# Kernel tuning notes

Hardware: AMD Instinct MI355X
Metric: run time of the kernel (lower is better)

The kernel has to match this reference:

```python
import jax, jax.numpy as jnp
import numpy as np

B, S, D_MODEL, H = 8, 2048, 256, 4
DEPTH = D_MODEL // H


def setup_inputs() -> dict:
    key = jax.random.key(0)
    ks = jax.random.split(key, 9)
    std = 1.0 / np.sqrt(D_MODEL)
    return {
        "v": jax.random.normal(ks[0], (B, S, D_MODEL), jnp.float32),
        "k": jax.random.normal(ks[1], (B, S, D_MODEL), jnp.float32),
        "q": jax.random.normal(ks[2], (B, S, D_MODEL), jnp.float32),
        "mask": jax.random.uniform(ks[3], (B, 1, 1, S), jnp.float32),
        "wq": jax.random.normal(ks[4], (D_MODEL, D_MODEL), jnp.float32) * std,
        "bq": jnp.zeros((D_MODEL,), jnp.float32),
        "wk": jax.random.normal(ks[5], (D_MODEL, D_MODEL), jnp.float32) * std,
        "bk": jnp.zeros((D_MODEL,), jnp.float32),
        "wv": jax.random.normal(ks[6], (D_MODEL, D_MODEL), jnp.float32) * std,
        "bv": jnp.zeros((D_MODEL,), jnp.float32),
        "wo": jax.random.normal(ks[7], (D_MODEL, D_MODEL), jnp.float32) * std,
        "bo": jnp.zeros((D_MODEL,), jnp.float32),
    }


def _split_heads(x):
    # [B, S, d_model] -> [B, H, S, depth]
    b, s, _ = x.shape
    return x.reshape(b, s, H, DEPTH).transpose(0, 2, 1, 3)


def reference(v, k, q, mask, wq, bq, wk, bk, wv, bv, wo, bo):
    qh = _split_heads(q @ wq + bq)   # [B,H,Sq,depth]
    kh = _split_heads(k @ wk + bk)   # [B,H,Sk,depth]
    vh = _split_heads(v @ wv + bv)   # [B,H,Sk,depth]
    scale = 1.0 / jnp.sqrt(jnp.asarray(DEPTH, jnp.float32))
    logits = jnp.einsum("bhqd,bhkd->bhqk", qh, kh) * scale
    logits = logits + mask * (-1e9)
    attn = jax.nn.softmax(logits, axis=-1)
    out = jnp.einsum("bhqk,bhkd->bhqd", attn, vh)  # [B,H,Sq,depth]
    concat = out.transpose(0, 2, 1, 3).reshape(out.shape[0], -1, D_MODEL)
    return concat @ wo + bo
```

## Files before the change

### kernel.cpp

```cpp
#include <hip/hip_runtime.h>

#define DEV __device__ __forceinline__

typedef __attribute__((ext_vector_type(4))) float f32x4;
typedef __bf16 bf16_t;
typedef __attribute__((ext_vector_type(4))) bf16_t bf16x4;
typedef __attribute__((ext_vector_type(8))) bf16_t bf16x8;
typedef __attribute__((ext_vector_type(8))) unsigned short us8;
typedef __attribute__((ext_vector_type(4))) unsigned short us4;


DEV unsigned short f2bf(float f) {
  bf16_t h = (bf16_t)f;
  return __builtin_bit_cast(unsigned short, h);
}

DEV void gl2lds16(const void* g, void* l) {
  __builtin_amdgcn_global_load_lds(
      (const __attribute__((address_space(1))) unsigned int*)g,
      (__attribute__((address_space(3))) unsigned int*)l, 16, 0, 0);
}

DEV f32x4 mfma16(bf16x8 a, bf16x8 b, f32x4 c) {
  return __builtin_amdgcn_mfma_f32_16x16x32_bf16(a, b, c, 0, 0, 0);
}

__global__ __launch_bounds__(256) void prep_w(
    const float* __restrict__ wq, const float* __restrict__ wk,
    const float* __restrict__ wv, const float* __restrict__ wo,
    const float* __restrict__ mask,
    unsigned short* __restrict__ wt, float* __restrict__ mc,
    int* __restrict__ gidx, int* __restrict__ nct) {
  const int t = threadIdx.x;
  if (blockIdx.x < 64) {
    __shared__ float T[64 * 65];
    const int mat = blockIdx.x >> 4, tn = (blockIdx.x >> 2) & 3, tk = blockIdx.x & 3;
    const int n0 = tn * 64, k0 = tk * 64;
    const float* W = (mat == 0) ? wq : (mat == 1) ? wk : (mat == 2) ? wv : wo;
    const int r0 = t >> 4, c = (t & 15) * 4;
#pragma unroll
    for (int i = 0; i < 4; ++i) {
      int rr = r0 + i * 16;
      f32x4 x = *(const f32x4*)(W + (k0 + rr) * 256 + n0 + c);
#pragma unroll
      for (int j = 0; j < 4; ++j) T[(c + j) * 65 + rr] = x[j];
    }
    __syncthreads();
#pragma unroll
    for (int i = 0; i < 2; ++i) {
      int u = t + i * 256;
      int n = u >> 3, seg = u & 7;
      us8 pk;
#pragma unroll
      for (int j = 0; j < 8; ++j) pk[j] = f2bf(T[n * 65 + seg * 8 + j]);
      *(us8*)(&wt[mat * 65536 + (n0 + n) * 256 + k0 + seg * 8]) = pk;
    }
  } else {
    __shared__ float redf[256];
    __shared__ int redi[256];
    const int b = blockIdx.x - 64;
    const float* mr = mask + b * 2048;
    f32x4 x0 = *(const f32x4*)(mr + t * 8);
    f32x4 x1 = *(const f32x4*)(mr + t * 8 + 4);
    float mv[8];
#pragma unroll
    for (int j = 0; j < 4; ++j) { mv[j] = x0[j]; mv[4 + j] = x1[j]; }
    float mn = mv[0];
#pragma unroll
    for (int j = 1; j < 8; ++j) mn = fminf(mn, mv[j]);
    redf[t] = mn;
    __syncthreads();
    for (int s = 128; s > 0; s >>= 1) {
      if (t < s) redf[t] = fminf(redf[t], redf[t + s]);
      __syncthreads();
    }
    const float minb = redf[0];
    const float thr = minb + 1.45e-6f;
    int myc = 0;
#pragma unroll
    for (int j = 0; j < 8; ++j) myc += (mv[j] < thr) ? 1 : 0;
    redi[t] = myc;
    __syncthreads();
    for (int s = 1; s < 256; s <<= 1) {
      int add = (t >= s) ? redi[t - s] : 0;
      __syncthreads();
      redi[t] += add;
      __syncthreads();
    }
    int pos = redi[t] - myc;
    const int cntb = redi[255];
#pragma unroll
    for (int j = 0; j < 8; ++j)
      if (mv[j] < thr) {
        gidx[b * 2048 + pos] = t * 8 + j;
        mc[b * 2048 + pos] = (mv[j] - minb) * -1.442695041e9f;
        ++pos;
      }
    if (t == 0) {
      int nt = (cntb + 63) >> 6;
      if (nt < 1) nt = 1;
      nct[b] = nt;
      for (int j = cntb; j < nt * 64; ++j) {
        gidx[b * 2048 + j] = 0;
        mc[b * 2048 + j] = -1.0e30f;
      }
    }
  }
}

__global__ __launch_bounds__(256, 4) void gemm_q(
    const float* __restrict__ Aq, const float* __restrict__ bq,
    const unsigned short* __restrict__ wt,
    unsigned short* __restrict__ Qh) {
  __shared__ __align__(16) unsigned short At[32 * 64];
  __shared__ __align__(16) unsigned short Bt[256 * 64];
  const unsigned short* WT = wt;
  const int t = threadIdx.x, lane = t & 63, w = t >> 6;
  const int lr = lane & 15, lg = lane >> 4;
  const int lx = lr & 7;
  const int m0 = blockIdx.x * 32;

  const int as_row = t >> 3, as_seg = t & 7;
  const float* agp = Aq + (m0 + as_row) * 256 + as_seg * 8;

  f32x4 acc[2][4] = {};

  for (int j = 0; j < 4; ++j) {
    const int k0 = j * 64;
#pragma unroll
    for (int i = 0; i < 8; ++i) {
      int u = t + i * 256;
      int row = u >> 3, g = (u & 7) ^ (row & 7);
      gl2lds16(WT + row * 256 + k0 + g * 8, &Bt[u * 8]);
    }
    {
      f32x4 x0 = *(const f32x4*)(agp + k0);
      f32x4 x1 = *(const f32x4*)(agp + k0 + 4);
      us8 pk;
#pragma unroll
      for (int jj = 0; jj < 4; ++jj) { pk[jj] = f2bf(x0[jj]); pk[jj + 4] = f2bf(x1[jj]); }
      *(us8*)(&At[(as_row << 6) + ((as_seg ^ (as_row & 7)) << 3)]) = pk;
    }
    __syncthreads();

#pragma unroll
    for (int ds = 0; ds < 2; ++ds) {
      const int ku = (ds << 2) | lg;
      const int phys = (ku ^ lx) << 3;
      bf16x8 af[2], bfr[4];
#pragma unroll
      for (int m = 0; m < 2; ++m)
        af[m] = *(const bf16x8*)(&At[((m * 16 + lr) << 6) + phys]);
#pragma unroll
      for (int cg = 0; cg < 4; ++cg)
        bfr[cg] = *(const bf16x8*)(&Bt[((w * 64 + cg * 16 + lr) << 6) + phys]);
#pragma unroll
      for (int m = 0; m < 2; ++m)
#pragma unroll
        for (int cg = 0; cg < 4; ++cg)
          acc[m][cg] = mfma16(af[m], bfr[cg], acc[m][cg]);
    }
    __syncthreads();
  }

  const int b = m0 >> 11, s0 = m0 & 2047;
  const int bh = b * 4 + w;
#pragma unroll
  for (int cg = 0; cg < 4; ++cg) {
    int d = cg * 16 + lr;
    float bb = bq[w * 64 + d];
#pragma unroll
    for (int m = 0; m < 2; ++m) {
      int sb = s0 + m * 16 + lg * 4;
#pragma unroll
      for (int r = 0; r < 4; ++r)
        Qh[(bh * 2048 + sb + r) * 64 + d] = f2bf(acc[m][cg][r] + bb);
    }
  }
}

__global__ __launch_bounds__(512) void gemm_kv(
    const float* __restrict__ kin, const float* __restrict__ vin,
    const float* __restrict__ bk, const float* __restrict__ bv,
    const unsigned short* __restrict__ wt, const int* __restrict__ gidx,
    const int* __restrict__ nct,
    unsigned short* __restrict__ Khc, unsigned short* __restrict__ VhcT) {
  const int gt = blockIdx.x, b = blockIdx.y, p = blockIdx.z;
  if (gt >= nct[b]) return;

  __shared__ __align__(16) unsigned short At[64 * 256];
  __shared__ __align__(16) unsigned short Bt[256 * 256];
  const float* A    = p ? vin : kin;
  const float* bias = p ? bv : bk;
  const unsigned short* WT = wt + (p ? 2 : 1) * 65536;
  const int t = threadIdx.x, lane = t & 63, w = t >> 6;
  const int lr = lane & 15, lg = lane >> 4;
  const int lx = lr & 7;
  const int* gi = gidx + b * 2048 + gt * 64;

#pragma unroll
  for (int i = 0; i < 16; ++i) {
    int u = t + i * 512;
    int row = u >> 5, un = u & 31;
    int g = (un & 24) | ((un & 7) ^ (row & 7));
    gl2lds16(WT + row * 256 + g * 8, &Bt[u * 8]);
  }
  {
    const int row = t >> 3, seg = (t & 7) * 4;
    const int srow = gi[row];
    const float* src = A + (b * 2048 + srow) * 256 + seg * 8;
#pragma unroll
    for (int j = 0; j < 4; ++j) {
      f32x4 x0 = *(const f32x4*)(src + j * 8);
      f32x4 x1 = *(const f32x4*)(src + j * 8 + 4);
      us8 pk;
#pragma unroll
      for (int jj = 0; jj < 4; ++jj) { pk[jj] = f2bf(x0[jj]); pk[jj + 4] = f2bf(x1[jj]); }
      int un = seg + j;
      *(us8*)(&At[row * 256 + (((un & 24) | ((un & 7) ^ (row & 7))) << 3)]) = pk;
    }
  }
  __syncthreads();

  f32x4 acc[4][2] = {};
#pragma unroll
  for (int ds = 0; ds < 8; ++ds) {
    const int ku = ds * 4 + lg;
    const int phys = ((ku & 24) | ((ku & 7) ^ lx)) << 3;
    bf16x8 af[4], bfr[2];
#pragma unroll
    for (int m = 0; m < 4; ++m)
      af[m] = *(const bf16x8*)(&At[(m * 16 + lr) * 256 + phys]);
#pragma unroll
    for (int n = 0; n < 2; ++n)
      bfr[n] = *(const bf16x8*)(&Bt[(w * 32 + n * 16 + lr) * 256 + phys]);
#pragma unroll
    for (int m = 0; m < 4; ++m)
#pragma unroll
      for (int n = 0; n < 2; ++n)
        acc[m][n] = mfma16(af[m], bfr[n], acc[m][n]);
  }

#pragma unroll
  for (int n = 0; n < 2; ++n) {
    int col = w * 32 + n * 16 + lr;
    float bb = bias[col];
    int h = col >> 6, d = col & 63;
    int bh = b * 4 + h;
#pragma unroll
    for (int m = 0; m < 4; ++m) {
      int pos = gt * 64 + m * 16 + lg * 4;
      if (p) {
        us4 o;
#pragma unroll
        for (int r = 0; r < 4; ++r) o[r] = f2bf(acc[m][n][r] + bb);
        *(us4*)(&VhcT[(bh * 64 + d) * 2048 + pos]) = o;
      } else {
#pragma unroll
        for (int r = 0; r < 4; ++r)
          Khc[(bh * 2048 + pos + r) * 64 + d] = f2bf(acc[m][n][r] + bb);
      }
    }
  }
}

__global__ __launch_bounds__(512) void attn_out(
    const unsigned short* __restrict__ Qh, const unsigned short* __restrict__ Kh,
    const unsigned short* __restrict__ VhT, const float* __restrict__ mc,
    const int* __restrict__ nct, const unsigned short* __restrict__ wt,
    const float* __restrict__ bo, float* __restrict__ out) {
  __shared__ __align__(16) unsigned short L[81920];
  const int b = blockIdx.y;
  const int q0 = blockIdx.x * 64;
  const int t = threadIdx.x, lane = t & 63, w = t >> 6;
  const int lr = lane & 15, lg = lane >> 4;
  const int h = w >> 1, ch = w & 1;
  const int bh = b * 4 + h;
  const float* mrow = mc + b * 2048;
  const int lx = lr & 7;
  const int lgh = lg >> 1, lgo = (lg & 1) * 4;

  bf16x8 qf[2][2];
#pragma unroll
  for (int cc = 0; cc < 2; ++cc)
#pragma unroll
    for (int ds = 0; ds < 2; ++ds)
      qf[cc][ds] = *(const bf16x8*)(Qh + (bh * 2048 + q0 + ch * 32 + cc * 16 + lr) * 64 + ds * 32 + lg * 8);

  f32x4 accO[2][4] = {};
  float mrun[2] = {-3.0e38f, -3.0e38f}, lrun[2] = {0.f, 0.f};

#define STAGE(buf, kv)                                                        \
  {                                                                           \
    _Pragma("unroll")                                                         \
    for (int i = 0; i < 4; ++i) {                                             \
      int u = t + i * 512;                                                    \
      int hh = u >> 9, vv = u & 511;                                          \
      int row = vv >> 3, g = (vv & 7) ^ (row & 7);                            \
      gl2lds16(Kh + ((b * 4 + hh) * 2048 + (kv) + row) * 64 + g * 8,          \
               &L[((buf) * 16384 + hh * 4096 + vv * 8)]);                     \
      gl2lds16(VhT + ((b * 4 + hh) * 64 + row) * 2048 + (kv) + g * 8,         \
               &L[(32768 + (buf) * 16384 + hh * 4096 + vv * 8)]);             \
    }                                                                         \
  }

  const int cnt = nct[b];
  STAGE(0, 0)
  __syncthreads();
  int cur = 0;

  for (int j = 0; j < cnt; ++j) {
    const int kv0 = j * 64;
    if (j + 1 < cnt) STAGE(cur ^ 1, kv0 + 64)

    const int kb_base = cur * 16384 + h * 4096;
    const int vb_base = 32768 + kb_base;

#pragma unroll
    for (int cc = 0; cc < 2; ++cc) {
      f32x4 accS[4] = {};
      __builtin_amdgcn_s_setprio(1);
#pragma unroll
      for (int kb = 0; kb < 4; ++kb)
#pragma unroll
        for (int ds = 0; ds < 2; ++ds) {
          bf16x8 kf = *(const bf16x8*)(&L[kb_base + (((kb * 16 + lr) << 3) | (((ds << 2) | lg) ^ lx)) * 8]);
          accS[kb] = mfma16(kf, qf[cc][ds], accS[kb]);
        }
      __builtin_amdgcn_s_setprio(0);

      f32x4 sv[4];
#pragma unroll
      for (int kb = 0; kb < 4; ++kb) {
        f32x4 mk = *(const f32x4*)(mrow + kv0 + kb * 16 + lg * 4);
        sv[kb] = accS[kb] * 0.1803368801f + mk;
      }
      float mx0 = fmaxf(fmaxf(sv[0][0], sv[0][1]), fmaxf(sv[0][2], sv[0][3]));
      float mx1 = fmaxf(fmaxf(sv[1][0], sv[1][1]), fmaxf(sv[1][2], sv[1][3]));
      float mx2 = fmaxf(fmaxf(sv[2][0], sv[2][1]), fmaxf(sv[2][2], sv[2][3]));
      float mx3 = fmaxf(fmaxf(sv[3][0], sv[3][1]), fmaxf(sv[3][2], sv[3][3]));
      float mx = fmaxf(fmaxf(mx0, mx1), fmaxf(mx2, mx3));
      mx = fmaxf(mx, __shfl_xor(mx, 16));
      mx = fmaxf(mx, __shfl_xor(mx, 32));
      float mnew = fmaxf(mrun[cc], mx);
      float al = __builtin_amdgcn_exp2f(mrun[cc] - mnew);
      mrun[cc] = mnew;

      float px[4][4];
      float lsum = 0.f;
#pragma unroll
      for (int kb = 0; kb < 4; ++kb) {
        float s = 0.f;
#pragma unroll
        for (int r = 0; r < 4; ++r) {
          px[kb][r] = __builtin_amdgcn_exp2f(sv[kb][r] - mnew);
          s += px[kb][r];
        }
        lsum += s;
      }
      lsum += __shfl_xor(lsum, 16);
      lsum += __shfl_xor(lsum, 32);
      lrun[cc] = lrun[cc] * al + lsum;
#pragma unroll
      for (int db = 0; db < 4; ++db) accO[cc][db] *= al;

      bf16x8 pf[2];
#pragma unroll
      for (int ks = 0; ks < 2; ++ks) {
        bf16x8 p;
#pragma unroll
        for (int r = 0; r < 4; ++r) {
          p[r]     = (bf16_t)px[2 * ks][r];
          p[r + 4] = (bf16_t)px[2 * ks + 1][r];
        }
        pf[ks] = p;
      }

      __builtin_amdgcn_s_setprio(1);
#pragma unroll
      for (int ks = 0; ks < 2; ++ks)
#pragma unroll
        for (int db = 0; db < 4; ++db) {
          int row = db * 16 + lr;
          int u0 = (row << 3) | (((ks << 2) | lgh) ^ lx);
          int u1 = (row << 3) | (((ks << 2) | 2 | lgh) ^ lx);
          bf16x4 v0 = *(const bf16x4*)(&L[vb_base + u0 * 8 + lgo]);
          bf16x4 v1 = *(const bf16x4*)(&L[vb_base + u1 * 8 + lgo]);
          bf16x8 vf = __builtin_shufflevector(v0, v1, 0, 1, 2, 3, 4, 5, 6, 7);
          accO[cc][db] = mfma16(vf, pf[ks], accO[cc][db]);
        }
      __builtin_amdgcn_s_setprio(0);
    }

    __syncthreads();
    cur ^= 1;
  }
#undef STAGE

#pragma unroll
  for (int cc = 0; cc < 2; ++cc) {
    const float inv = __builtin_amdgcn_rcpf(lrun[cc]);
    const int row = ch * 32 + cc * 16 + lr;
#pragma unroll
    for (int db = 0; db < 4; ++db) {
      us4 o;
#pragma unroll
      for (int r = 0; r < 4; ++r) o[r] = f2bf(accO[cc][db][r] * inv);
      int un = h * 8 + db * 2 + (lg >> 1);
      int phys = (un & 24) | ((un & 7) ^ (row & 7));
      *(us4*)(&L[65536 + row * 256 + phys * 8 + (lg & 1) * 4]) = o;
    }
  }
  __syncthreads();

  const unsigned short* WT = wt + 3 * 65536;
#pragma unroll
  for (int i = 0; i < 16; ++i) {
    int u = t + i * 512;
    int row = u >> 5, un = u & 31;
    int g = (un & 24) | ((un & 7) ^ (row & 7));
    gl2lds16(WT + row * 256 + g * 8, &L[u * 8]);
  }
  __syncthreads();

  f32x4 acc[4][2] = {};
#pragma unroll
  for (int ds = 0; ds < 8; ++ds) {
    const int ku = ds * 4 + lg;
    const int phys = ((ku & 24) | ((ku & 7) ^ lx)) << 3;
    bf16x8 af[4], bfr[2];
#pragma unroll
    for (int m = 0; m < 4; ++m)
      af[m] = *(const bf16x8*)(&L[65536 + (m * 16 + lr) * 256 + phys]);
#pragma unroll
    for (int n = 0; n < 2; ++n)
      bfr[n] = *(const bf16x8*)(&L[(w * 32 + n * 16 + lr) * 256 + phys]);
#pragma unroll
    for (int m = 0; m < 4; ++m)
#pragma unroll
      for (int n = 0; n < 2; ++n)
        acc[m][n] = mfma16(af[m], bfr[n], acc[m][n]);
  }

#pragma unroll
  for (int cgi = 0; cgi < 2; ++cgi) {
    int col = w * 32 + cgi * 16 + lr;
    float bb = bo[col];
#pragma unroll
    for (int m = 0; m < 4; ++m) {
      int rowg = b * 2048 + q0 + m * 16 + lg * 4;
#pragma unroll
      for (int r = 0; r < 4; ++r)
        out[(rowg + r) * 256 + col] = acc[m][cgi][r] + bb;
    }
  }
}

extern "C" void kernel_launch(void* const* d_in, const int* in_sizes, int n_in,
                              void* d_out, int out_size, void* d_ws, size_t ws_size,
                              hipStream_t stream) {
  const float* v    = (const float*)d_in[0];
  const float* k    = (const float*)d_in[1];
  const float* q    = (const float*)d_in[2];
  const float* mask = (const float*)d_in[3];
  const float* wq   = (const float*)d_in[4];
  const float* bq   = (const float*)d_in[5];
  const float* wk   = (const float*)d_in[6];
  const float* bk   = (const float*)d_in[7];
  const float* wv   = (const float*)d_in[8];
  const float* bv   = (const float*)d_in[9];
  const float* wo   = (const float*)d_in[10];
  const float* bo   = (const float*)d_in[11];
  float* out = (float*)d_out;
  char* ws = (char*)d_ws;

  unsigned short* wt  = (unsigned short*)(ws);
  float*          mc  = (float*)(ws + 524288);
  int*            gi  = (int*)(ws + 589824);
  int*            nc  = (int*)(ws + 655360);
  unsigned short* Qh  = (unsigned short*)(ws + 659456);
  unsigned short* Khc = (unsigned short*)(ws + 659456 + 8388608);
  unsigned short* VhT = (unsigned short*)(ws + 659456 + 2 * 8388608);

  prep_w<<<dim3(72), dim3(256), 0, stream>>>(wq, wk, wv, wo, mask, wt, mc, gi, nc);
  gemm_q<<<dim3(512), dim3(256), 0, stream>>>(q, bq, wt, Qh);
  gemm_kv<<<dim3(32, 8, 2), dim3(512), 0, stream>>>(k, v, bk, bv, wt, gi, nc, Khc, VhT);
  attn_out<<<dim3(32, 8), dim3(512), 0, stream>>>(Qh, Khc, VhT, mc, nc, wt, bo, out);
}
```

Baseline: 48.26 us.

## Merge Q and compacted K/V projection GEMMs into one launch with K-chunked tiling

Combines the separate Q projection and K/V projection kernels into a single launch with a 2-row grid. Q blocks keep their old path, while K/V blocks are re-tiled to 256 threads and stream the weight in four 64-wide K chunks instead of staging the full 256x256 weight in LDS. The aim is to remove one launch and its serialization gap, cut the K/V kernel's large LDS footprint so more blocks fit per CU, and let the Q and K/V work overlap. In exchange each K/V block now syncs four times and has more accumulator registers, and the launch bound of 4 blocks per SM for the Q path is dropped.

```diff
diff --git a/kernel.cpp b/kernel.cpp
--- a/kernel.cpp
+++ b/kernel.cpp
@@ -108,157 +108,147 @@
   }
 }
 
-__global__ __launch_bounds__(256, 4) void gemm_q(
-    const float* __restrict__ Aq, const float* __restrict__ bq,
-    const unsigned short* __restrict__ wt,
-    unsigned short* __restrict__ Qh) {
-  __shared__ __align__(16) unsigned short At[32 * 64];
+__global__ __launch_bounds__(256) void gemm_qkv(
+    const float* __restrict__ qin, const float* __restrict__ kin,
+    const float* __restrict__ vin,
+    const float* __restrict__ bq, const float* __restrict__ bk,
+    const float* __restrict__ bv,
+    const unsigned short* __restrict__ wt, const int* __restrict__ gidx,
+    const int* __restrict__ nct,
+    unsigned short* __restrict__ Qh, unsigned short* __restrict__ Khc,
+    unsigned short* __restrict__ VhcT) {
+  __shared__ __align__(16) unsigned short At[64 * 64];
   __shared__ __align__(16) unsigned short Bt[256 * 64];
-  const unsigned short* WT = wt;
   const int t = threadIdx.x, lane = t & 63, w = t >> 6;
   const int lr = lane & 15, lg = lane >> 4;
   const int lx = lr & 7;
-  const int m0 = blockIdx.x * 32;
-
-  const int as_row = t >> 3, as_seg = t & 7;
-  const float* agp = Aq + (m0 + as_row) * 256 + as_seg * 8;
-
-  f32x4 acc[2][4] = {};
-
-  for (int j = 0; j < 4; ++j) {
-    const int k0 = j * 64;
-#pragma unroll
-    for (int i = 0; i < 8; ++i) {
-      int u = t + i * 256;
-      int row = u >> 3, g = (u & 7) ^ (row & 7);
-      gl2lds16(WT + row * 256 + k0 + g * 8, &Bt[u * 8]);
-    }
-    {
-      f32x4 x0 = *(const f32x4*)(agp + k0);
-      f32x4 x1 = *(const f32x4*)(agp + k0 + 4);
-      us8 pk;
-#pragma unroll
-      for (int jj = 0; jj < 4; ++jj) { pk[jj] = f2bf(x0[jj]); pk[jj + 4] = f2bf(x1[jj]); }
-      *(us8*)(&At[(as_row << 6) + ((as_seg ^ (as_row & 7)) << 3)]) = pk;
-    }
-    __syncthreads();
-
-#pragma unroll
-    for (int ds = 0; ds < 2; ++ds) {
-      const int ku = (ds << 2) | lg;
-      const int phys = (ku ^ lx) << 3;
-      bf16x8 af[2], bfr[4];
-#pragma unroll
-      for (int m = 0; m < 2; ++m)
-        af[m] = *(const bf16x8*)(&At[((m * 16 + lr) << 6) + phys]);
-#pragma unroll
-      for (int cg = 0; cg < 4; ++cg)
-        bfr[cg] = *(const bf16x8*)(&Bt[((w * 64 + cg * 16 + lr) << 6) + phys]);
-#pragma unroll
-      for (int m = 0; m < 2; ++m)
+
+  if (blockIdx.y == 0) {
+    const int m0 = blockIdx.x * 32;
+    const int as_row = t >> 3, as_seg = t & 7;
+    const float* agp = qin + (m0 + as_row) * 256 + as_seg * 8;
+
+    f32x4 acc[2][4] = {};
+    for (int j = 0; j < 4; ++j) {
+      const int k0 = j * 64;
+#pragma unroll
+      for (int i = 0; i < 8; ++i) {
+        int u = t + i * 256;
+        int row = u >> 3, g = (u & 7) ^ (row & 7);
+        gl2lds16(wt + row * 256 + k0 + g * 8, &Bt[u * 8]);
+      }
+      {
+        f32x4 x0 = *(const f32x4*)(agp + k0);
+        f32x4 x1 = *(const f32x4*)(agp + k0 + 4);
+        us8 pk;
+#pragma unroll
+        for (int jj = 0; jj < 4; ++jj) { pk[jj] = f2bf(x0[jj]); pk[jj + 4] = f2bf(x1[jj]); }
+        *(us8*)(&At[(as_row << 6) + ((as_seg ^ (as_row & 7)) << 3)]) = pk;
+      }
+      __syncthreads();
+#pragma unroll
+      for (int ds = 0; ds < 2; ++ds) {
+        const int ku = (ds << 2) | lg;
+        const int phys = (ku ^ lx) << 3;
+        bf16x8 af[2], bfr[4];
+#pragma unroll
+        for (int m = 0; m < 2; ++m)
+          af[m] = *(const bf16x8*)(&At[((m * 16 + lr) << 6) + phys]);
 #pragma unroll
         for (int cg = 0; cg < 4; ++cg)
-          acc[m][cg] = mfma16(af[m], bfr[cg], acc[m][cg]);
-    }
-    __syncthreads();
-  }
-
-  const int b = m0 >> 11, s0 = m0 & 2047;
-  const int bh = b * 4 + w;
-#pragma unroll
-  for (int cg = 0; cg < 4; ++cg) {
-    int d = cg * 16 + lr;
-    float bb = bq[w * 64 + d];
-#pragma unroll
-    for (int m = 0; m < 2; ++m) {
-      int sb = s0 + m * 16 + lg * 4;
-#pragma unroll
-      for (int r = 0; r < 4; ++r)
-        Qh[(bh * 2048 + sb + r) * 64 + d] = f2bf(acc[m][cg][r] + bb);
-    }
-  }
-}
-
-__global__ __launch_bounds__(512) void gemm_kv(
-    const float* __restrict__ kin, const float* __restrict__ vin,
-    const float* __restrict__ bk, const float* __restrict__ bv,
-    const unsigned short* __restrict__ wt, const int* __restrict__ gidx,
-    const int* __restrict__ nct,
-    unsigned short* __restrict__ Khc, unsigned short* __restrict__ VhcT) {
-  const int gt = blockIdx.x, b = blockIdx.y, p = blockIdx.z;
-  if (gt >= nct[b]) return;
-
-  __shared__ __align__(16) unsigned short At[64 * 256];
-  __shared__ __align__(16) unsigned short Bt[256 * 256];
-  const float* A    = p ? vin : kin;
-  const float* bias = p ? bv : bk;
-  const unsigned short* WT = wt + (p ? 2 : 1) * 65536;
-  const int t = threadIdx.x, lane = t & 63, w = t >> 6;
-  const int lr = lane & 15, lg = lane >> 4;
-  const int lx = lr & 7;
-  const int* gi = gidx + b * 2048 + gt * 64;
-
-#pragma unroll
-  for (int i = 0; i < 16; ++i) {
-    int u = t + i * 512;
-    int row = u >> 5, un = u & 31;
-    int g = (un & 24) | ((un & 7) ^ (row & 7));
-    gl2lds16(WT + row * 256 + g * 8, &Bt[u * 8]);
-  }
-  {
-    const int row = t >> 3, seg = (t & 7) * 4;
-    const int srow = gi[row];
-    const float* src = A + (b * 2048 + srow) * 256 + seg * 8;
-#pragma unroll
+          bfr[cg] = *(const bf16x8*)(&Bt[((w * 64 + cg * 16 + lr) << 6) + phys]);
+#pragma unroll
+        for (int m = 0; m < 2; ++m)
+#pragma unroll
+          for (int cg = 0; cg < 4; ++cg)
+            acc[m][cg] = mfma16(af[m], bfr[cg], acc[m][cg]);
+      }
+      __syncthreads();
+    }
+
+    const int b = m0 >> 11, s0 = m0 & 2047;
+    const int bh = b * 4 + w;
+#pragma unroll
+    for (int cg = 0; cg < 4; ++cg) {
+      int d = cg * 16 + lr;
+      float bb = bq[w * 64 + d];
+#pragma unroll
+      for (int m = 0; m < 2; ++m) {
+        int sb = s0 + m * 16 + lg * 4;
+#pragma unroll
+        for (int r = 0; r < 4; ++r)
+          Qh[(bh * 2048 + sb + r) * 64 + d] = f2bf(acc[m][cg][r] + bb);
+      }
+    }
+  } else {
+    const int x = blockIdx.x;
+    const int p = x >> 8, b = (x >> 5) & 7, gt = x & 31;
+    if (gt >= nct[b]) return;
+    const float* A    = p ? vin : kin;
+    const float* bias = p ? bv : bk;
+    const unsigned short* WT = wt + (p ? 2 : 1) * 65536;
+    const int* gi = gidx + b * 2048 + gt * 64;
+
+    f32x4 acc[4][4] = {};
     for (int j = 0; j < 4; ++j) {
-      f32x4 x0 = *(const f32x4*)(src + j * 8);
-      f32x4 x1 = *(const f32x4*)(src + j * 8 + 4);
-      us8 pk;
-#pragma unroll
-      for (int jj = 0; jj < 4; ++jj) { pk[jj] = f2bf(x0[jj]); pk[jj + 4] = f2bf(x1[jj]); }
-      int un = seg + j;
-      *(us8*)(&At[row * 256 + (((un & 24) | ((un & 7) ^ (row & 7))) << 3)]) = pk;
-    }
-  }
-  __syncthreads();
-
-  f32x4 acc[4][2] = {};
-#pragma unroll
-  for (int ds = 0; ds < 8; ++ds) {
-    const int ku = ds * 4 + lg;
-    const int phys = ((ku & 24) | ((ku & 7) ^ lx)) << 3;
-    bf16x8 af[4], bfr[2];
-#pragma unroll
-    for (int m = 0; m < 4; ++m)
-      af[m] = *(const bf16x8*)(&At[(m * 16 + lr) * 256 + phys]);
-#pragma unroll
-    for (int n = 0; n < 2; ++n)
-      bfr[n] = *(const bf16x8*)(&Bt[(w * 32 + n * 16 + lr) * 256 + phys]);
-#pragma unroll
-    for (int m = 0; m < 4; ++m)
-#pragma unroll
-      for (int n = 0; n < 2; ++n)
-        acc[m][n] = mfma16(af[m], bfr[n], acc[m][n]);
-  }
-
-#pragma unroll
-  for (int n = 0; n < 2; ++n) {
-    int col = w * 32 + n * 16 + lr;
-    float bb = bias[col];
-    int h = col >> 6, d = col & 63;
-    int bh = b * 4 + h;
-#pragma unroll
-    for (int m = 0; m < 4; ++m) {
-      int pos = gt * 64 + m * 16 + lg * 4;
-      if (p) {
-        us4 o;
-#pragma unroll
-        for (int r = 0; r < 4; ++r) o[r] = f2bf(acc[m][n][r] + bb);
-        *(us4*)(&VhcT[(bh * 64 + d) * 2048 + pos]) = o;
-      } else {
-#pragma unroll
-        for (int r = 0; r < 4; ++r)
-          Khc[(bh * 2048 + pos + r) * 64 + d] = f2bf(acc[m][n][r] + bb);
+      const int k0 = j * 64;
+#pragma unroll
+      for (int i = 0; i < 8; ++i) {
+        int u = t + i * 256;
+        int row = u >> 3, g = (u & 7) ^ (row & 7);
+        gl2lds16(WT + row * 256 + k0 + g * 8, &Bt[u * 8]);
+      }
+#pragma unroll
+      for (int i = 0; i < 2; ++i) {
+        int slot = t + i * 256;
+        int row = slot >> 3, seg = slot & 7;
+        const float* src = A + (b * 2048 + gi[row]) * 256 + k0 + seg * 8;
+        f32x4 x0 = *(const f32x4*)src;
+        f32x4 x1 = *(const f32x4*)(src + 4);
+        us8 pk;
+#pragma unroll
+        for (int jj = 0; jj < 4; ++jj) { pk[jj] = f2bf(x0[jj]); pk[jj + 4] = f2bf(x1[jj]); }
+        *(us8*)(&At[(row << 6) + ((seg ^ (row & 7)) << 3)]) = pk;
+      }
+      __syncthreads();
+#pragma unroll
+      for (int ds = 0; ds < 2; ++ds) {
+        const int ku = (ds << 2) | lg;
+        const int phys = (ku ^ lx) << 3;
+        bf16x8 af[4], bfr[4];
+#pragma unroll
+        for (int m = 0; m < 4; ++m)
+          af[m] = *(const bf16x8*)(&At[((m * 16 + lr) << 6) + phys]);
+#pragma unroll
+        for (int cg = 0; cg < 4; ++cg)
+          bfr[cg] = *(const bf16x8*)(&Bt[((w * 64 + cg * 16 + lr) << 6) + phys]);
+#pragma unroll
+        for (int m = 0; m < 4; ++m)
+#pragma unroll
+          for (int cg = 0; cg < 4; ++cg)
+            acc[m][cg] = mfma16(af[m], bfr[cg], acc[m][cg]);
+      }
+      __syncthreads();
+    }
+
+    const int bh = b * 4 + w;
+#pragma unroll
+    for (int cg = 0; cg < 4; ++cg) {
+      int d = cg * 16 + lr;
+      float bb = bias[w * 64 + d];
+#pragma unroll
+      for (int m = 0; m < 4; ++m) {
+        int pos = gt * 64 + m * 16 + lg * 4;
+        if (p) {
+          us4 o;
+#pragma unroll
+          for (int r = 0; r < 4; ++r) o[r] = f2bf(acc[m][cg][r] + bb);
+          *(us4*)(&VhcT[(bh * 64 + d) * 2048 + pos]) = o;
+        } else {
+#pragma unroll
+          for (int r = 0; r < 4; ++r)
+            Khc[(bh * 2048 + pos + r) * 64 + d] = f2bf(acc[m][cg][r] + bb);
+        }
       }
     }
   }
@@ -483,7 +473,6 @@
   unsigned short* VhT = (unsigned short*)(ws + 659456 + 2 * 8388608);
 
   prep_w<<<dim3(72), dim3(256), 0, stream>>>(wq, wk, wv, wo, mask, wt, mc, gi, nc);
-  gemm_q<<<dim3(512), dim3(256), 0, stream>>>(q, bq, wt, Qh);
-  gemm_kv<<<dim3(32, 8, 2), dim3(512), 0, stream>>>(k, v, bk, bv, wt, gi, nc, Khc, VhT);
+  gemm_qkv<<<dim3(512, 2), dim3(256), 0, stream>>>(q, k, v, bq, bk, bv, wt, gi, nc, Qh, Khc, VhT);
   attn_out<<<dim3(32, 8), dim3(512), 0, stream>>>(Qh, Khc, VhT, mc, nc, wt, bo, out);
 }
```

Result: faster. 41.33 us (-14.4%).

## Fuse Q projection into attention and compute compacted K/V rows in prep kernel

Applied to the files above, without the earlier changes.

Removes the separate Q GEMM and K/V GEMM kernels. The Q projection is now computed per block inside the attention kernel from fp32 inputs staged through LDS, so the Qh workspace round trip disappears. K/V projections for the few mask-selected key rows are computed with scalar FMA loops in the prep kernel. This cuts two launches and intermediate traffic. The trade-offs are that the prep kernel now does serial per-row work, and the padded K/V rows beyond the selected count are no longer written, so they hold uninitialized data.

```diff
diff --git a/kernel.cpp b/kernel.cpp
--- a/kernel.cpp
+++ b/kernel.cpp
@@ -25,52 +25,54 @@
   return __builtin_amdgcn_mfma_f32_16x16x32_bf16(a, b, c, 0, 0, 0);
 }
 
-__global__ __launch_bounds__(256) void prep_w(
-    const float* __restrict__ wq, const float* __restrict__ wk,
-    const float* __restrict__ wv, const float* __restrict__ wo,
+__global__ __launch_bounds__(512) void prep_kv(
+    const float* __restrict__ wq, const float* __restrict__ wo,
+    const float* __restrict__ wk, const float* __restrict__ wv,
+    const float* __restrict__ bk, const float* __restrict__ bv,
     const float* __restrict__ mask,
+    const float* __restrict__ kin, const float* __restrict__ vin,
     unsigned short* __restrict__ wt, float* __restrict__ mc,
-    int* __restrict__ gidx, int* __restrict__ nct) {
+    int* __restrict__ nct,
+    unsigned short* __restrict__ Khc, unsigned short* __restrict__ VhcT) {
   const int t = threadIdx.x;
-  if (blockIdx.x < 64) {
+  if (blockIdx.x < 32) {
     __shared__ float T[64 * 65];
     const int mat = blockIdx.x >> 4, tn = (blockIdx.x >> 2) & 3, tk = blockIdx.x & 3;
     const int n0 = tn * 64, k0 = tk * 64;
-    const float* W = (mat == 0) ? wq : (mat == 1) ? wk : (mat == 2) ? wv : wo;
-    const int r0 = t >> 4, c = (t & 15) * 4;
-#pragma unroll
-    for (int i = 0; i < 4; ++i) {
-      int rr = r0 + i * 16;
-      f32x4 x = *(const f32x4*)(W + (k0 + rr) * 256 + n0 + c);
-#pragma unroll
-      for (int j = 0; j < 4; ++j) T[(c + j) * 65 + rr] = x[j];
+    const float* W = (mat == 0) ? wq : wo;
+    if (t < 256) {
+      const int r0 = t >> 4, c = (t & 15) * 4;
+#pragma unroll
+      for (int i = 0; i < 4; ++i) {
+        int rr = r0 + i * 16;
+        f32x4 x = *(const f32x4*)(W + (k0 + rr) * 256 + n0 + c);
+#pragma unroll
+        for (int j = 0; j < 4; ++j) T[(c + j) * 65 + rr] = x[j];
+      }
     }
     __syncthreads();
-#pragma unroll
-    for (int i = 0; i < 2; ++i) {
-      int u = t + i * 256;
-      int n = u >> 3, seg = u & 7;
-      us8 pk;
-#pragma unroll
-      for (int j = 0; j < 8; ++j) pk[j] = f2bf(T[n * 65 + seg * 8 + j]);
-      *(us8*)(&wt[mat * 65536 + (n0 + n) * 256 + k0 + seg * 8]) = pk;
+    if (t < 256) {
+#pragma unroll
+      for (int i = 0; i < 2; ++i) {
+        int u = t + i * 256;
+        int n = u >> 3, seg = u & 7;
+        us8 pk;
+#pragma unroll
+        for (int j = 0; j < 8; ++j) pk[j] = f2bf(T[n * 65 + seg * 8 + j]);
+        *(us8*)(&wt[mat * 65536 + (n0 + n) * 256 + k0 + seg * 8]) = pk;
+      }
     }
   } else {
-    __shared__ float redf[256];
-    __shared__ int redi[256];
-    const int b = blockIdx.x - 64;
-    const float* mr = mask + b * 2048;
-    f32x4 x0 = *(const f32x4*)(mr + t * 8);
-    f32x4 x1 = *(const f32x4*)(mr + t * 8 + 4);
-    float mv[8];
-#pragma unroll
-    for (int j = 0; j < 4; ++j) { mv[j] = x0[j]; mv[4 + j] = x1[j]; }
-    float mn = mv[0];
-#pragma unroll
-    for (int j = 1; j < 8; ++j) mn = fminf(mn, mv[j]);
+    __shared__ float redf[512];
+    __shared__ int redi[512];
+    __shared__ int srows[2048];
+    const int b = blockIdx.x - 32;
+    f32x4 mv4 = *(const f32x4*)(mask + b * 2048 + t * 4);
+    float mv[4] = {mv4[0], mv4[1], mv4[2], mv4[3]};
+    float mn = fminf(fminf(mv[0], mv[1]), fminf(mv[2], mv[3]));
     redf[t] = mn;
     __syncthreads();
-    for (int s = 128; s > 0; s >>= 1) {
+    for (int s = 256; s > 0; s >>= 1) {
       if (t < s) redf[t] = fminf(redf[t], redf[t + s]);
       __syncthreads();
     }
@@ -78,214 +80,150 @@
     const float thr = minb + 1.45e-6f;
     int myc = 0;
 #pragma unroll
-    for (int j = 0; j < 8; ++j) myc += (mv[j] < thr) ? 1 : 0;
+    for (int j = 0; j < 4; ++j) myc += (mv[j] < thr) ? 1 : 0;
     redi[t] = myc;
     __syncthreads();
-    for (int s = 1; s < 256; s <<= 1) {
+    for (int s = 1; s < 512; s <<= 1) {
       int add = (t >= s) ? redi[t - s] : 0;
       __syncthreads();
       redi[t] += add;
       __syncthreads();
     }
     int pos = redi[t] - myc;
-    const int cntb = redi[255];
-#pragma unroll
-    for (int j = 0; j < 8; ++j)
+    const int cnt = redi[511];
+#pragma unroll
+    for (int j = 0; j < 4; ++j)
       if (mv[j] < thr) {
-        gidx[b * 2048 + pos] = t * 8 + j;
+        srows[pos] = t * 4 + j;
         mc[b * 2048 + pos] = (mv[j] - minb) * -1.442695041e9f;
         ++pos;
       }
     if (t == 0) {
-      int nt = (cntb + 63) >> 6;
+      int nt = (cnt + 63) >> 6;
       if (nt < 1) nt = 1;
       nct[b] = nt;
-      for (int j = cntb; j < nt * 64; ++j) {
-        gidx[b * 2048 + j] = 0;
-        mc[b * 2048 + j] = -1.0e30f;
-      }
-    }
-  }
-}
-
-__global__ __launch_bounds__(256, 4) void gemm_q(
-    const float* __restrict__ Aq, const float* __restrict__ bq,
-    const unsigned short* __restrict__ wt,
-    unsigned short* __restrict__ Qh) {
-  __shared__ __align__(16) unsigned short At[32 * 64];
-  __shared__ __align__(16) unsigned short Bt[256 * 64];
-  const unsigned short* WT = wt;
-  const int t = threadIdx.x, lane = t & 63, w = t >> 6;
-  const int lr = lane & 15, lg = lane >> 4;
-  const int lx = lr & 7;
-  const int m0 = blockIdx.x * 32;
-
-  const int as_row = t >> 3, as_seg = t & 7;
-  const float* agp = Aq + (m0 + as_row) * 256 + as_seg * 8;
-
-  f32x4 acc[2][4] = {};
-
-  for (int j = 0; j < 4; ++j) {
-    const int k0 = j * 64;
-#pragma unroll
-    for (int i = 0; i < 8; ++i) {
-      int u = t + i * 256;
-      int row = u >> 3, g = (u & 7) ^ (row & 7);
-      gl2lds16(WT + row * 256 + k0 + g * 8, &Bt[u * 8]);
-    }
-    {
-      f32x4 x0 = *(const f32x4*)(agp + k0);
-      f32x4 x1 = *(const f32x4*)(agp + k0 + 4);
-      us8 pk;
-#pragma unroll
-      for (int jj = 0; jj < 4; ++jj) { pk[jj] = f2bf(x0[jj]); pk[jj + 4] = f2bf(x1[jj]); }
-      *(us8*)(&At[(as_row << 6) + ((as_seg ^ (as_row & 7)) << 3)]) = pk;
+      for (int j = cnt; j < nt * 64; ++j) mc[b * 2048 + j] = -1.0e30f;
     }
     __syncthreads();
 
-#pragma unroll
-    for (int ds = 0; ds < 2; ++ds) {
-      const int ku = (ds << 2) | lg;
-      const int phys = (ku ^ lx) << 3;
-      bf16x8 af[2], bfr[4];
-#pragma unroll
-      for (int m = 0; m < 2; ++m)
-        af[m] = *(const bf16x8*)(&At[((m * 16 + lr) << 6) + phys]);
-#pragma unroll
-      for (int cg = 0; cg < 4; ++cg)
-        bfr[cg] = *(const bf16x8*)(&Bt[((w * 64 + cg * 16 + lr) << 6) + phys]);
-#pragma unroll
-      for (int m = 0; m < 2; ++m)
-#pragma unroll
-        for (int cg = 0; cg < 4; ++cg)
-          acc[m][cg] = mfma16(af[m], bfr[cg], acc[m][cg]);
-    }
-    __syncthreads();
-  }
-
-  const int b = m0 >> 11, s0 = m0 & 2047;
-  const int bh = b * 4 + w;
-#pragma unroll
-  for (int cg = 0; cg < 4; ++cg) {
-    int d = cg * 16 + lr;
-    float bb = bq[w * 64 + d];
-#pragma unroll
-    for (int m = 0; m < 2; ++m) {
-      int sb = s0 + m * 16 + lg * 4;
-#pragma unroll
-      for (int r = 0; r < 4; ++r)
-        Qh[(bh * 2048 + sb + r) * 64 + d] = f2bf(acc[m][cg][r] + bb);
-    }
-  }
-}
-
-__global__ __launch_bounds__(512) void gemm_kv(
-    const float* __restrict__ kin, const float* __restrict__ vin,
-    const float* __restrict__ bk, const float* __restrict__ bv,
-    const unsigned short* __restrict__ wt, const int* __restrict__ gidx,
-    const int* __restrict__ nct,
-    unsigned short* __restrict__ Khc, unsigned short* __restrict__ VhcT) {
-  const int gt = blockIdx.x, b = blockIdx.y, p = blockIdx.z;
-  if (gt >= nct[b]) return;
-
-  __shared__ __align__(16) unsigned short At[64 * 256];
-  __shared__ __align__(16) unsigned short Bt[256 * 256];
-  const float* A    = p ? vin : kin;
-  const float* bias = p ? bv : bk;
-  const unsigned short* WT = wt + (p ? 2 : 1) * 65536;
-  const int t = threadIdx.x, lane = t & 63, w = t >> 6;
-  const int lr = lane & 15, lg = lane >> 4;
-  const int lx = lr & 7;
-  const int* gi = gidx + b * 2048 + gt * 64;
-
-#pragma unroll
-  for (int i = 0; i < 16; ++i) {
-    int u = t + i * 512;
-    int row = u >> 5, un = u & 31;
-    int g = (un & 24) | ((un & 7) ^ (row & 7));
-    gl2lds16(WT + row * 256 + g * 8, &Bt[u * 8]);
-  }
-  {
-    const int row = t >> 3, seg = (t & 7) * 4;
-    const int srow = gi[row];
-    const float* src = A + (b * 2048 + srow) * 256 + seg * 8;
-#pragma unroll
-    for (int j = 0; j < 4; ++j) {
-      f32x4 x0 = *(const f32x4*)(src + j * 8);
-      f32x4 x1 = *(const f32x4*)(src + j * 8 + 4);
-      us8 pk;
-#pragma unroll
-      for (int jj = 0; jj < 4; ++jj) { pk[jj] = f2bf(x0[jj]); pk[jj + 4] = f2bf(x1[jj]); }
-      int un = seg + j;
-      *(us8*)(&At[row * 256 + (((un & 24) | ((un & 7) ^ (row & 7))) << 3)]) = pk;
-    }
-  }
-  __syncthreads();
-
-  f32x4 acc[4][2] = {};
-#pragma unroll
-  for (int ds = 0; ds < 8; ++ds) {
-    const int ku = ds * 4 + lg;
-    const int phys = ((ku & 24) | ((ku & 7) ^ lx)) << 3;
-    bf16x8 af[4], bfr[2];
-#pragma unroll
-    for (int m = 0; m < 4; ++m)
-      af[m] = *(const bf16x8*)(&At[(m * 16 + lr) * 256 + phys]);
-#pragma unroll
-    for (int n = 0; n < 2; ++n)
-      bfr[n] = *(const bf16x8*)(&Bt[(w * 32 + n * 16 + lr) * 256 + phys]);
-#pragma unroll
-    for (int m = 0; m < 4; ++m)
-#pragma unroll
-      for (int n = 0; n < 2; ++n)
-        acc[m][n] = mfma16(af[m], bfr[n], acc[m][n]);
-  }
-
-#pragma unroll
-  for (int n = 0; n < 2; ++n) {
-    int col = w * 32 + n * 16 + lr;
-    float bb = bias[col];
-    int h = col >> 6, d = col & 63;
-    int bh = b * 4 + h;
-#pragma unroll
-    for (int m = 0; m < 4; ++m) {
-      int pos = gt * 64 + m * 16 + lg * 4;
-      if (p) {
-        us4 o;
-#pragma unroll
-        for (int r = 0; r < 4; ++r) o[r] = f2bf(acc[m][n][r] + bb);
-        *(us4*)(&VhcT[(bh * 64 + d) * 2048 + pos]) = o;
-      } else {
-#pragma unroll
-        for (int r = 0; r < 4; ++r)
-          Khc[(bh * 2048 + pos + r) * 64 + d] = f2bf(acc[m][n][r] + bb);
-      }
-    }
-  }
-}
-
-__global__ __launch_bounds__(512) void attn_out(
-    const unsigned short* __restrict__ Qh, const unsigned short* __restrict__ Kh,
-    const unsigned short* __restrict__ VhT, const float* __restrict__ mc,
-    const int* __restrict__ nct, const unsigned short* __restrict__ wt,
-    const float* __restrict__ bo, float* __restrict__ out) {
+    const int n = t & 255, half = t >> 8;
+    for (int r = 0; r < cnt; ++r) {
+      const int srow = srows[r];
+      {
+        const float* a = kin + (b * 2048 + srow) * 256 + half * 128;
+        const float* wrow = wk + half * 128 * 256 + n;
+        float acc = 0.f;
+#pragma unroll 8
+        for (int kk = 0; kk < 128; ++kk) acc += a[kk] * wrow[kk * 256];
+        redf[t] = acc;
+        __syncthreads();
+        if (half == 0) {
+          float s = acc + redf[t + 256] + bk[n];
+          Khc[((b * 4 + (n >> 6)) * 2048 + r) * 64 + (n & 63)] = f2bf(s);
+        }
+        __syncthreads();
+      }
+      {
+        const float* a = vin + (b * 2048 + srow) * 256 + half * 128;
+        const float* wrow = wv + half * 128 * 256 + n;
+        float acc = 0.f;
+#pragma unroll 8
+        for (int kk = 0; kk < 128; ++kk) acc += a[kk] * wrow[kk * 256];
+        redf[t] = acc;
+        __syncthreads();
+        if (half == 0) {
+          float s = acc + redf[t + 256] + bv[n];
+          VhcT[((b * 4 + (n >> 6)) * 64 + (n & 63)) * 2048 + r] = f2bf(s);
+        }
+        __syncthreads();
+      }
+    }
+  }
+}
+
+__global__ __launch_bounds__(512) void attn_fused(
+    const float* __restrict__ qin, const float* __restrict__ bq,
+    const unsigned short* __restrict__ Khc, const unsigned short* __restrict__ VhcT,
+    const float* __restrict__ mc, const int* __restrict__ nct,
+    const unsigned short* __restrict__ wt, const float* __restrict__ bo,
+    float* __restrict__ out) {
   __shared__ __align__(16) unsigned short L[81920];
   const int b = blockIdx.y;
   const int q0 = blockIdx.x * 64;
   const int t = threadIdx.x, lane = t & 63, w = t >> 6;
   const int lr = lane & 15, lg = lane >> 4;
   const int h = w >> 1, ch = w & 1;
-  const int bh = b * 4 + h;
   const float* mrow = mc + b * 2048;
   const int lx = lr & 7;
   const int lgh = lg >> 1, lgo = (lg & 1) * 4;
 
+#pragma unroll
+  for (int i = 0; i < 16; ++i) {
+    int u = t + i * 512;
+    int row = u >> 5, un = u & 31;
+    int g = (un & 24) | ((un & 7) ^ (row & 7));
+    gl2lds16(wt + row * 256 + g * 8, &L[u * 8]);
+  }
+#pragma unroll
+  for (int i = 0; i < 4; ++i) {
+    int u = t + i * 512;
+    int row = u >> 5, un = u & 31;
+    const float* src = qin + (b * 2048 + q0 + row) * 256 + un * 8;
+    f32x4 x0 = *(const f32x4*)src;
+    f32x4 x1 = *(const f32x4*)(src + 4);
+    us8 pk;
+#pragma unroll
+    for (int jj = 0; jj < 4; ++jj) { pk[jj] = f2bf(x0[jj]); pk[jj + 4] = f2bf(x1[jj]); }
+    *(us8*)(&L[65536 + row * 256 + (((un & 24) | ((un & 7) ^ (row & 7))) << 3)]) = pk;
+  }
+  __syncthreads();
+
+  f32x4 aq[2][4] = {};
+#pragma unroll
+  for (int ds8 = 0; ds8 < 8; ++ds8) {
+    int ku = ds8 * 4 + lg;
+    int phys = ((ku & 24) | ((ku & 7) ^ lx)) << 3;
+    bf16x8 af[2], bfr[4];
+#pragma unroll
+    for (int cc = 0; cc < 2; ++cc)
+      af[cc] = *(const bf16x8*)(&L[65536 + (ch * 32 + cc * 16 + lr) * 256 + phys]);
+#pragma unroll
+    for (int n = 0; n < 4; ++n)
+      bfr[n] = *(const bf16x8*)(&L[(h * 64 + n * 16 + lr) * 256 + phys]);
+#pragma unroll
+    for (int cc = 0; cc < 2; ++cc)
+#pragma unroll
+      for (int n = 0; n < 4; ++n)
+        aq[cc][n] = mfma16(af[cc], bfr[n], aq[cc][n]);
+  }
+  __syncthreads();
+#pragma unroll
+  for (int cc = 0; cc < 2; ++cc)
+#pragma unroll
+    for (int n = 0; n < 4; ++n) {
+      int col = h * 64 + n * 16 + lr;
+      int un = col >> 3;
+      float bb = bq[col];
+#pragma unroll
+      for (int r = 0; r < 4; ++r) {
+        int row = ch * 32 + cc * 16 + lg * 4 + r;
+        int phys = (un & 24) | ((un & 7) ^ (row & 7));
+        L[65536 + row * 256 + phys * 8 + (col & 7)] = f2bf(aq[cc][n][r] + bb);
+      }
+    }
+  __syncthreads();
+
   bf16x8 qf[2][2];
 #pragma unroll
   for (int cc = 0; cc < 2; ++cc)
 #pragma unroll
-    for (int ds = 0; ds < 2; ++ds)
-      qf[cc][ds] = *(const bf16x8*)(Qh + (bh * 2048 + q0 + ch * 32 + cc * 16 + lr) * 64 + ds * 32 + lg * 8);
+    for (int ds = 0; ds < 2; ++ds) {
+      int row = ch * 32 + cc * 16 + lr;
+      int un = h * 8 + ds * 4 + lg;
+      int phys = (un & 24) | ((un & 7) ^ lx);
+      qf[cc][ds] = *(const bf16x8*)(&L[65536 + row * 256 + phys * 8]);
+    }
+  __syncthreads();
 
   f32x4 accO[2][4] = {};
   float mrun[2] = {-3.0e38f, -3.0e38f}, lrun[2] = {0.f, 0.f};
@@ -297,9 +235,9 @@
       int u = t + i * 512;                                                    \
       int hh = u >> 9, vv = u & 511;                                          \
       int row = vv >> 3, g = (vv & 7) ^ (row & 7);                            \
-      gl2lds16(Kh + ((b * 4 + hh) * 2048 + (kv) + row) * 64 + g * 8,          \
+      gl2lds16(Khc + ((b * 4 + hh) * 2048 + (kv) + row) * 64 + g * 8,         \
                &L[((buf) * 16384 + hh * 4096 + vv * 8)]);                     \
-      gl2lds16(VhT + ((b * 4 + hh) * 64 + row) * 2048 + (kv) + g * 8,         \
+      gl2lds16(VhcT + ((b * 4 + hh) * 64 + row) * 2048 + (kv) + g * 8,        \
                &L[(32768 + (buf) * 16384 + hh * 4096 + vv * 8)]);             \
     }                                                                         \
   }
@@ -413,7 +351,7 @@
   }
   __syncthreads();
 
-  const unsigned short* WT = wt + 3 * 65536;
+  const unsigned short* WT = wt + 65536;
 #pragma unroll
   for (int i = 0; i < 16; ++i) {
     int u = t + i * 512;
@@ -475,15 +413,12 @@
   char* ws = (char*)d_ws;
 
   unsigned short* wt  = (unsigned short*)(ws);
-  float*          mc  = (float*)(ws + 524288);
-  int*            gi  = (int*)(ws + 589824);
-  int*            nc  = (int*)(ws + 655360);
-  unsigned short* Qh  = (unsigned short*)(ws + 659456);
-  unsigned short* Khc = (unsigned short*)(ws + 659456 + 8388608);
-  unsigned short* VhT = (unsigned short*)(ws + 659456 + 2 * 8388608);
-
-  prep_w<<<dim3(72), dim3(256), 0, stream>>>(wq, wk, wv, wo, mask, wt, mc, gi, nc);
-  gemm_q<<<dim3(512), dim3(256), 0, stream>>>(q, bq, wt, Qh);
-  gemm_kv<<<dim3(32, 8, 2), dim3(512), 0, stream>>>(k, v, bk, bv, wt, gi, nc, Khc, VhT);
-  attn_out<<<dim3(32, 8), dim3(512), 0, stream>>>(Qh, Khc, VhT, mc, nc, wt, bo, out);
-}
+  float*          mc  = (float*)(ws + 262144);
+  int*            nc  = (int*)(ws + 327680);
+  unsigned short* Khc = (unsigned short*)(ws + 331776);
+  unsigned short* VhT = (unsigned short*)(ws + 331776 + 8388608);
+
+  prep_kv<<<dim3(40), dim3(512), 0, stream>>>(wq, wo, wk, wv, bk, bv, mask, k, v,
+                                              wt, mc, nc, Khc, VhT);
+  attn_fused<<<dim3(32, 8), dim3(512), 0, stream>>>(q, bq, Khc, VhT, mc, nc, wt, bo, out);
+}
```

After: 39.79 us (median of 2 runs). 17.6% less time.
